# Kernel optimization log

Measured on AMD Instinct MI355X. Metric: run time of the kernel, lower is better.

Reference implementation:

```python
import jax, jax.numpy as jnp
import numpy as np
from jax import lax


def setup_inputs() -> dict:
    key = jax.random.key(0)
    k1, k2, k3 = jax.random.split(key, 3)
    H = W = 2048
    K, p = 16, 15
    x = jax.random.uniform(k1, (1, 1, H, W), dtype=jnp.float32)
    patterns = jax.random.uniform(k2, (K, p, p), dtype=jnp.float32)
    vectors = jax.random.normal(k3, (K, 2), dtype=jnp.float32)
    return {"x": x, "patterns": patterns, "vectors": vectors}


def reference(x, patterns, vectors):
    K, p, _ = patterns.shape
    img = x[0, 0]                      # [H, W]
    H, W = img.shape
    # GENEO_1: pad by p on all sides; window at (i,j) covers padded [i:i+p, j:j+p]
    padded = jnp.pad(img, p)           # [H+2p, W+2p]
    ones_k = jnp.ones((1, 1, p, p), dtype=img.dtype)
    win_sum = lax.conv_general_dilated(
        padded[None, None], ones_k, window_strides=(1, 1), padding='VALID'
    )[0, 0]                            # [H+p+1, W+p+1]
    win_sum = win_sum[:H, :W]          # windows for i in [0,H), j in [0,W)
    # out[k,i,j] = 1 - (sum(pattern_k) - win_sum)/(p*p)
    pat_sum = patterns.sum(axis=(1, 2))                     # [K]
    F_k = 1.0 - (pat_sum[:, None, None] - win_sum[None]) / (p * p)  # [K,H,W]
    # GENEO_3: gather at (i - floor(vx), j - floor(vy)), torch negative-index wrap -> mod
    off = jnp.floor(vectors).astype(jnp.int32)              # [K,2]
    ri = (jnp.arange(H)[None, :] - off[:, 0:1]) % H          # [K,H]
    rj = (jnp.arange(W)[None, :] - off[:, 1:2]) % W          # [K,W]
    gathered = F_k[jnp.arange(K)[:, None, None], ri[:, :, None], rj[:, None, :]]  # [K,H,W]
    # original divides by final loop variable k == K-1 (faithful)
    out = gathered.sum(axis=0) / (K - 1)
    return out
```

## Files before the change

### kernel.cpp

```cpp
#include <hip/hip_runtime.h>
#include <math.h>

#define H 2048
#define W 2048
#define K 16
#define P 15
#define WP 2052
#define LDSP 272

typedef float v4 __attribute__((ext_vector_type(4)));
typedef v4 uv4 __attribute__((aligned(4)));

__global__ __launch_bounds__(320) void geneo_win(
        const float* __restrict__ img,
        float* __restrict__ win,
        const float* __restrict__ patterns,
        const float* __restrict__ vectors,
        float* __restrict__ consts,
        int* __restrict__ offs) {
    __shared__ float sl[48][LDSP];
    __shared__ float psum[5];
    int t  = threadIdx.x;
    int c0 = blockIdx.x * 256;
    int r0 = blockIdx.y * 32;

    if (blockIdx.x == 0 && blockIdx.y == 0) {
        float ps = 0.f;
        for (int idx = t; idx < 900; idx += 320) {
            v4 v = *(const v4*)&patterns[idx * 4];
            ps += (v.x + v.y) + (v.z + v.w);
        }
        #pragma unroll
        for (int d = 32; d > 0; d >>= 1) ps += __shfl_down(ps, d, 64);
        if ((t & 63) == 0) psum[t >> 6] = ps;
        if (t < 2 * K) offs[t] = (int)floorf(vectors[t]);
        __syncthreads();
        if (t == 0) {
            float total = ((psum[0] + psum[1]) + (psum[2] + psum[3])) + psum[4];
            consts[0] = (16.0f - total * (1.0f / 225.0f)) * (1.0f / 15.0f);
        }
    }

    for (int idx = t; idx < 47 * 68; idx += 320) {
        int q = idx / 68;
        int c = idx - q * 68;
        int grow = r0 - 15 + q;
        int gcol = c0 - 16 + 4 * c;
        v4 v = {0.f, 0.f, 0.f, 0.f};
        if (grow >= 0 && gcol >= 0)
            v = *(const v4*)&img[grow * W + gcol];
        *(v4*)&sl[q + 1][4 * c] = v;
    }
    __syncthreads();

    if (t < LDSP) {
        float s = 0.f;
        #pragma unroll
        for (int q = 1; q <= 15; ++q) s += sl[q][t];
        #pragma unroll
        for (int ii = 0; ii < 32; ++ii) {
            float sv = s;
            s += sl[ii + 16][t] - sl[ii + 1][t];
            sl[ii][t] = sv;
        }
    }
    __syncthreads();

    if (t < 256) {
        int gj = c0 + t;
        #pragma unroll 4
        for (int ii = 0; ii < 32; ++ii) {
            float s = 0.f;
            #pragma unroll
            for (int m = 1; m <= 15; ++m) s += sl[ii][t + m];
            int gi = r0 + ii;
            win[gi * WP + gj] = s;
            if (c0 == 0 && t < 4)
                win[gi * WP + 2048 + t] = s;
        }
    }
}

__global__ __launch_bounds__(256) void geneo_gather(
        const float* __restrict__ win,
        const float* __restrict__ consts,
        const int* __restrict__ offs,
        float* __restrict__ out) {
    __shared__ int soy[K], sox[K];
    __shared__ float sC;
    int t = threadIdx.x;
    if (t < K) { soy[t] = offs[t * 2]; sox[t] = offs[t * 2 + 1]; }
    if (t == 0) sC = consts[0];
    __syncthreads();

    int d   = blockIdx.x;
    int i   = ((d & 7) << 8) | (d >> 3);
    int j   = 4 * t;

    const float S = 1.0f / 3375.0f;
    v4 acc0 = {0.f, 0.f, 0.f, 0.f};
    v4 acc1 = {0.f, 0.f, 0.f, 0.f};
    #pragma unroll
    for (int k = 0; k < K; ++k) {
        int ri = (i - soy[k]) & (H - 1);
        int rj = (j - sox[k]) & (W - 1);
        const float* row = &win[ri * WP];
        acc0 += *(const uv4*)&row[rj];
        acc1 += *(const uv4*)&row[rj ^ 1024];
    }
    v4 o0 = acc0 * S + sC;
    v4 o1 = acc1 * S + sC;
    *(v4*)&out[i * W + j]        = o0;
    *(v4*)&out[i * W + j + 1024] = o1;
}

extern "C" void kernel_launch(void* const* d_in, const int* in_sizes, int n_in,
                              void* d_out, int out_size, void* d_ws, size_t ws_size,
                              hipStream_t stream) {
    const float* x        = (const float*)d_in[0];
    const float* patterns = (const float*)d_in[1];
    const float* vectors  = (const float*)d_in[2];
    float* out = (float*)d_out;

    float* win    = (float*)d_ws;
    float* consts = win + H * WP;
    int*   offs   = (int*)(consts + 1);

    geneo_win<<<dim3(8, 64), 320, 0, stream>>>(x, win, patterns, vectors, consts, offs);
    geneo_gather<<<2048, 256, 0, stream>>>(win, consts, offs, out);
}
```

Measured before the change: 93.51 us.

## Tile gather kernel through LDS with halo to reuse shifted window sums

The gather kernel now loads a 16x256 tile of window sums plus an 8-element halo into LDS, then accumulates all 16 shifted reads from LDS when an offset fits inside the halo. Offsets outside the halo fall back to wrapped global loads. This replaces 16 unaligned global vector loads per output with one cooperative tile load. The padded row stride and duplicated tail columns in the window kernel are removed. The catch is extra LDS traffic and a branch per k, and the fallback path is uncoalesced scalar loads if offsets are large.

```diff
diff --git a/kernel.cpp b/kernel.cpp
--- a/kernel.cpp
+++ b/kernel.cpp
@@ -5,11 +5,10 @@
 #define W 2048
 #define K 16
 #define P 15
-#define WP 2052
 #define LDSP 272
+#define HALO 8
 
 typedef float v4 __attribute__((ext_vector_type(4)));
-typedef v4 uv4 __attribute__((aligned(4)));
 
 __global__ __launch_bounds__(320) void geneo_win(
         const float* __restrict__ img,
@@ -31,7 +30,7 @@
             ps += (v.x + v.y) + (v.z + v.w);
         }
         #pragma unroll
-        for (int d = 32; d > 0; d >>= 1) ps += __shfl_down(ps, d, 64);
+        for (int q = 32; q > 0; q >>= 1) ps += __shfl_down(ps, q, 64);
         if ((t & 63) == 0) psum[t >> 6] = ps;
         if (t < 2 * K) offs[t] = (int)floorf(vectors[t]);
         __syncthreads();
@@ -72,11 +71,8 @@
         for (int ii = 0; ii < 32; ++ii) {
             float s = 0.f;
             #pragma unroll
-            for (int m = 1; m <= 15; ++m) s += sl[ii][t + m];
-            int gi = r0 + ii;
-            win[gi * WP + gj] = s;
-            if (c0 == 0 && t < 4)
-                win[gi * WP + 2048 + t] = s;
+            for (int mm = 1; mm <= 15; ++mm) s += sl[ii][t + mm];
+            win[(r0 + ii) * W + gj] = s;
         }
     }
 }
@@ -86,32 +82,63 @@
         const float* __restrict__ consts,
         const int* __restrict__ offs,
         float* __restrict__ out) {
+    __shared__ float sl[32][272];
     __shared__ int soy[K], sox[K];
     __shared__ float sC;
     int t = threadIdx.x;
     if (t < K) { soy[t] = offs[t * 2]; sox[t] = offs[t * 2 + 1]; }
     if (t == 0) sC = consts[0];
+
+    int d  = blockIdx.x;
+    int m  = d >> 3;
+    int r0 = ((d & 7) << 8) | ((m & 15) << 4);
+    int c0 = (m >> 4) << 8;
+
+    for (int idx = t; idx < 32 * 68; idx += 256) {
+        int q = idx / 68;
+        int c = idx - q * 68;
+        int gr = (r0 - HALO + q) & (H - 1);
+        int gc = (c0 - HALO + 4 * c) & (W - 1);
+        *(v4*)&sl[q][4 * c] = *(const v4*)&win[gr * W + gc];
+    }
     __syncthreads();
 
-    int d   = blockIdx.x;
-    int i   = ((d & 7) << 8) | (d >> 3);
-    int j   = 4 * t;
+    int w = t >> 6;
+    int l = t & 63;
+    float acc[4][4] = {{0.f}};
+    #pragma unroll
+    for (int k = 0; k < K; ++k) {
+        int dy = soy[k], dx = sox[k];
+        if (dy >= -HALO && dy <= HALO && dx >= -HALO && dx <= HALO) {
+            int lr = HALO + 4 * w - dy;
+            int lc = HALO + l - dx;
+            #pragma unroll
+            for (int r = 0; r < 4; ++r) {
+                const float* row = &sl[lr + r][lc];
+                #pragma unroll
+                for (int g = 0; g < 4; ++g) acc[r][g] += row[64 * g];
+            }
+        } else {
+            #pragma unroll
+            for (int r = 0; r < 4; ++r) {
+                int ri = (r0 + 4 * w + r - dy) & (H - 1);
+                #pragma unroll
+                for (int g = 0; g < 4; ++g) {
+                    int rj = (c0 + l + 64 * g - dx) & (W - 1);
+                    acc[r][g] += win[ri * W + rj];
+                }
+            }
+        }
+    }
 
     const float S = 1.0f / 3375.0f;
-    v4 acc0 = {0.f, 0.f, 0.f, 0.f};
-    v4 acc1 = {0.f, 0.f, 0.f, 0.f};
     #pragma unroll
-    for (int k = 0; k < K; ++k) {
-        int ri = (i - soy[k]) & (H - 1);
-        int rj = (j - sox[k]) & (W - 1);
-        const float* row = &win[ri * WP];
-        acc0 += *(const uv4*)&row[rj];
-        acc1 += *(const uv4*)&row[rj ^ 1024];
+    for (int r = 0; r < 4; ++r) {
+        int gi = r0 + 4 * w + r;
+        #pragma unroll
+        for (int g = 0; g < 4; ++g)
+            out[gi * W + c0 + 64 * g + l] = acc[r][g] * S + sC;
     }
-    v4 o0 = acc0 * S + sC;
-    v4 o1 = acc1 * S + sC;
-    *(v4*)&out[i * W + j]        = o0;
-    *(v4*)&out[i * W + j + 1024] = o1;
 }
 
 extern "C" void kernel_launch(void* const* d_in, const int* in_sizes, int n_in,
@@ -123,9 +150,9 @@
     float* out = (float*)d_out;
 
     float* win    = (float*)d_ws;
-    float* consts = win + H * WP;
+    float* consts = win + H * W;
     int*   offs   = (int*)(consts + 1);
 
     geneo_win<<<dim3(8, 64), 320, 0, stream>>>(x, win, patterns, vectors, consts, offs);
-    geneo_gather<<<2048, 256, 0, stream>>>(win, consts, offs, out);
+    geneo_gather<<<1024, 256, 0, stream>>>(win, consts, offs, out);
 }
```

Result: slower. 105.6 us (+12.9%).

## Sort gather offsets and compute horizontal window sums via width-5 partials

Applied to the files above, without the earlier changes.

The horizontal 15-wide sum is split into width-5 partial sums stored in spare LDS rows, then combined with three reads. This cuts LDS reads per output from 15 to about 8 at the cost of extra barriers and a staging pass. The offsets are also sorted by (row, column) on one thread, so the gather kernel visits rows in order, which may improve cache locality. The sort adds serial work inside block (0,0) of the window kernel.

```diff
diff --git a/kernel.cpp b/kernel.cpp
--- a/kernel.cpp
+++ b/kernel.cpp
@@ -31,9 +31,25 @@
             ps += (v.x + v.y) + (v.z + v.w);
         }
         #pragma unroll
-        for (int d = 32; d > 0; d >>= 1) ps += __shfl_down(ps, d, 64);
+        for (int q = 32; q > 0; q >>= 1) ps += __shfl_down(ps, q, 64);
         if ((t & 63) == 0) psum[t >> 6] = ps;
-        if (t < 2 * K) offs[t] = (int)floorf(vectors[t]);
+        if (t == 64) {
+            int oy[K], ox[K];
+            for (int k = 0; k < K; ++k) {
+                oy[k] = (int)floorf(vectors[2 * k]);
+                ox[k] = (int)floorf(vectors[2 * k + 1]);
+            }
+            for (int a = 1; a < K; ++a) {
+                int y = oy[a], x = ox[a], b = a - 1;
+                while (b >= 0 && (oy[b] > y || (oy[b] == y && ox[b] > x))) {
+                    oy[b + 1] = oy[b]; ox[b + 1] = ox[b]; --b;
+                }
+                oy[b + 1] = y; ox[b + 1] = x;
+            }
+            for (int k = 0; k < K; ++k) {
+                offs[2 * k] = oy[k]; offs[2 * k + 1] = ox[k];
+            }
+        }
         __syncthreads();
         if (t == 0) {
             float total = ((psum[0] + psum[1]) + (psum[2] + psum[3])) + psum[4];
@@ -64,19 +80,28 @@
             sl[ii][t] = sv;
         }
     }
-    __syncthreads();
 
-    if (t < 256) {
-        int gj = c0 + t;
-        #pragma unroll 4
-        for (int ii = 0; ii < 32; ++ii) {
-            float s = 0.f;
+    #pragma unroll
+    for (int b = 0; b < 32; b += 16) {
+        __syncthreads();
+        if (t < 268) {
             #pragma unroll
-            for (int m = 1; m <= 15; ++m) s += sl[ii][t + m];
-            int gi = r0 + ii;
-            win[gi * WP + gj] = s;
-            if (c0 == 0 && t < 4)
-                win[gi * WP + 2048 + t] = s;
+            for (int rr = 0; rr < 16; ++rr) {
+                const float* c = &sl[b + rr][t];
+                sl[32 + rr][t] = ((c[0] + c[1]) + (c[2] + c[3])) + c[4];
+            }
+        }
+        __syncthreads();
+        if (t < 256) {
+            #pragma unroll
+            for (int rr = 0; rr < 16; ++rr) {
+                const float* t5 = &sl[32 + rr][t];
+                float s = t5[1] + t5[6] + t5[11];
+                int gi = r0 + b + rr;
+                win[gi * WP + c0 + t] = s;
+                if (c0 == 0 && t < 4)
+                    win[gi * WP + 2048 + t] = s;
+            }
         }
     }
 }
@@ -93,9 +118,9 @@
     if (t == 0) sC = consts[0];
     __syncthreads();
 
-    int d   = blockIdx.x;
-    int i   = ((d & 7) << 8) | (d >> 3);
-    int j   = 4 * t;
+    int d = blockIdx.x;
+    int i = ((d & 7) << 8) | (d >> 3);
+    int j = 4 * t;
 
     const float S = 1.0f / 3375.0f;
     v4 acc0 = {0.f, 0.f, 0.f, 0.f};
```

Measured after the change: 104.5 us. 11.7% more time.
